# Kernel tuning notes

Hardware: AMD Instinct MI355X
Metric: run time of the kernel (lower is better)

Reference implementation:

```python
import jax, jax.numpy as jnp
import numpy as np

B, S, T = 64, 48, 48
E, H = 512, 1024
V_SRC, V_TGT = 32000, 32000
PAD = 0


def setup_inputs() -> dict:
    key = jax.random.key(0)
    ks = jax.random.split(key, 24)
    def g(k, shape, scale=0.05):
        return jax.random.normal(k, shape, dtype=jnp.float32) * scale
    return {
        "src_ids": jax.random.randint(ks[0], (S, B), 0, V_SRC),
        "tgt_ids": jax.random.randint(ks[1], (T, B), 0, V_TGT),
        "src_lengths": S,
        "src_emb": g(ks[2], (V_SRC, E)).at[PAD].set(0.0),
        "tgt_emb": g(ks[3], (V_TGT, E)).at[PAD].set(0.0),
        "cnn_w": g(ks[4], (E, E, 2)),
        "cnn_b": g(ks[5], (E,)),
        "enc_Wih_f": g(ks[6], (4 * H, E)),
        "enc_Whh_f": g(ks[7], (4 * H, H)),
        "enc_bih_f": g(ks[8], (4 * H,)),
        "enc_bhh_f": g(ks[9], (4 * H,)),
        "enc_Wih_b": g(ks[10], (4 * H, E)),
        "enc_Whh_b": g(ks[11], (4 * H, H)),
        "enc_bih_b": g(ks[12], (4 * H,)),
        "enc_bhh_b": g(ks[13], (4 * H,)),
        "dec_Wih": g(ks[14], (4 * H, E + H)),
        "dec_Whh": g(ks[15], (4 * H, H)),
        "dec_bih": g(ks[16], (4 * H,)),
        "dec_bhh": g(ks[17], (4 * H,)),
        "Wh": g(ks[18], (H, 2 * H)),
        "Wc": g(ks[19], (H, 2 * H)),
        "Watt": g(ks[20], (H, 2 * H)),
        "Wcomb": g(ks[21], (H, 3 * H)),
        "Wvocab": g(ks[22], (V_TGT, H)),
    }


def _lstm_cell(x, h, c, Wih, Whh, bih, bhh):
    gates = x @ Wih.T + h @ Whh.T + bih + bhh  # (b, 4h)
    i, f, g, o = jnp.split(gates, 4, axis=-1)
    c_new = jax.nn.sigmoid(f) * c + jax.nn.sigmoid(i) * jnp.tanh(g)
    h_new = jax.nn.sigmoid(o) * jnp.tanh(c_new)
    return h_new, c_new


def _forward(src_ids, tgt_ids,
             src_emb, tgt_emb, cnn_w, cnn_b,
             enc_Wih_f, enc_Whh_f, enc_bih_f, enc_bhh_f,
             enc_Wih_b, enc_Whh_b, enc_bih_b, enc_bhh_b,
             dec_Wih, dec_Whh, dec_bih, dec_bhh,
             Wh, Wc, Watt, Wcomb, Wvocab):
    b = src_ids.shape[1]
    h = Wh.shape[0]
    # ---- encode ----
    X = src_emb[src_ids]                       # (S, b, E)
    Xc = jnp.transpose(X, (1, 2, 0))           # (b, E, S)
    # Conv1d kernel_size=2, padding='same' in torch pads (left=0, right=1)
    Xc = jax.lax.conv_general_dilated(Xc, cnn_w, window_strides=(1,),
                                      padding=[(0, 1)],
                                      dimension_numbers=("NCH", "OIH", "NCH"))
    Xc = Xc + cnn_b[None, :, None]
    X = jnp.transpose(Xc, (2, 0, 1))           # (S, b, E)

    h0 = jnp.zeros((b, h), dtype=X.dtype)
    def fstep(carry, x_t):
        hh, cc = carry
        hh, cc = _lstm_cell(x_t, hh, cc, enc_Wih_f, enc_Whh_f, enc_bih_f, enc_bhh_f)
        return (hh, cc), hh
    def bstep(carry, x_t):
        hh, cc = carry
        hh, cc = _lstm_cell(x_t, hh, cc, enc_Wih_b, enc_Whh_b, enc_bih_b, enc_bhh_b)
        return (hh, cc), hh
    (hf, cf), out_f = jax.lax.scan(fstep, (h0, h0), X)
    (hb, cb), out_b = jax.lax.scan(bstep, (h0, h0), X[::-1])
    out_b = out_b[::-1]
    enc_hiddens = jnp.concatenate([out_f, out_b], axis=-1)   # (S, b, 2h)
    enc_hiddens = jnp.transpose(enc_hiddens, (1, 0, 2))      # (b, S, 2h)
    dec_h = jnp.concatenate([hf, hb], axis=1) @ Wh.T         # (b, h)
    dec_c = jnp.concatenate([cf, cb], axis=1) @ Wc.T         # (b, h)

    # ---- decode ----
    enc_proj = enc_hiddens @ Watt.T            # (b, S, h)
    enc_mask = jnp.zeros((b, enc_hiddens.shape[1]), dtype=bool)  # all full length
    Y = tgt_emb[tgt_ids[:-1]]                  # (T-1, b, E)

    def dstep(carry, Y_t):
        hh, cc, o_prev = carry
        ybar = jnp.concatenate([o_prev, Y_t], axis=1)        # (b, h+E)
        hh, cc = _lstm_cell(ybar, hh, cc, dec_Wih, dec_Whh, dec_bih, dec_bhh)
        e_t = jnp.einsum("bh,bsh->bs", hh, enc_proj)
        e_t = jnp.where(enc_mask, -jnp.inf, e_t)
        alpha = jax.nn.softmax(e_t, axis=-1)
        a_t = jnp.einsum("bs,bsd->bd", alpha, enc_hiddens)   # (b, 2h)
        O_t = jnp.tanh(jnp.concatenate([a_t, hh], axis=1) @ Wcomb.T)  # dropout rate 0
        return (hh, cc, O_t), O_t

    o0 = jnp.zeros((b, h), dtype=X.dtype)
    _, combined = jax.lax.scan(dstep, (dec_h, dec_c, o0), Y)  # (T-1, b, h)

    P = jax.nn.log_softmax(combined @ Wvocab.T, axis=-1)      # (T-1, b, V)
    gold = tgt_ids[1:]                                        # (T-1, b)
    logp = jnp.take_along_axis(P, gold[..., None], axis=-1)[..., 0]
    tmask = (gold != PAD).astype(P.dtype)
    return (logp * tmask).sum(axis=0)                         # (b,)


def reference(src_ids, tgt_ids, src_lengths,
              src_emb, tgt_emb, cnn_w, cnn_b,
              enc_Wih_f, enc_Whh_f, enc_bih_f, enc_bhh_f,
              enc_Wih_b, enc_Whh_b, enc_bih_b, enc_bhh_b,
              dec_Wih, dec_Whh, dec_bih, dec_bhh,
              Wh, Wc, Watt, Wcomb, Wvocab):
    # src_lengths == S for every sentence (packed seq degenerates to full-length LSTM)
    return _forward(src_ids, tgt_ids, src_emb, tgt_emb, cnn_w, cnn_b,
                    enc_Wih_f, enc_Whh_f, enc_bih_f, enc_bhh_f,
                    enc_Wih_b, enc_Whh_b, enc_bih_b, enc_bhh_b,
                    dec_Wih, dec_Whh, dec_bih, dec_bhh,
                    Wh, Wc, Watt, Wcomb, Wvocab)
```

## Files before the change

### kernel.cpp

```cpp
#include <hip/hip_runtime.h>
#include <hip/hip_bf16.h>
#include <math.h>

using f32x4 = __attribute__((ext_vector_type(4))) float;
using s16x8 = __attribute__((ext_vector_type(8))) short;
typedef unsigned short u16;
typedef unsigned int u32;
typedef unsigned long long u64;

#define MFMA16(a,b,c) __builtin_amdgcn_mfma_f32_16x16x32_bf16(a,b,c,0,0,0)
#define SCOPE_A __HIP_MEMORY_SCOPE_AGENT

__device__ __forceinline__ float bf2f(u16 u){
  union { u32 i; float f; } v; v.i = ((u32)u) << 16; return v.f;
}
__device__ __forceinline__ u16 f2bf(float f){
  union { float f; u32 i; } v; v.f = f;
  u32 x = v.i;
  return (u16)((x + 0x7fffu + ((x >> 16) & 1u)) >> 16);
}
__device__ __forceinline__ float sigm(float x){ return 1.0f/(1.0f + expf(-x)); }

__device__ __forceinline__ s16x8 pack8(const float* p){
  s16x8 r;
  #pragma unroll
  for (int i = 0; i < 8; ++i) r[i] = (short)f2bf(p[i]);
  return r;
}

__device__ __forceinline__ void coh_st32(void* p, u32 v){
  __hip_atomic_store((u32*)p, v, __ATOMIC_RELAXED, SCOPE_A);
}
__device__ __forceinline__ float u2f(u32 u){ union { u32 i; float f; } v; v.i = u; return v.f; }
__device__ __forceinline__ u32 f2u(float f){ union { float f; u32 i; } v; v.f = f; return v.i; }

__device__ __forceinline__ void poll(const int* flags, int n, int gen){
  for (int i = threadIdx.x; i < n; i += 256)
    while (__hip_atomic_load(flags + i, __ATOMIC_RELAXED, SCOPE_A) < gen)
      __builtin_amdgcn_s_sleep(1);
  __syncthreads();
}
__device__ __forceinline__ void setflag(int* flag, int gen){
  __syncthreads();
  if (threadIdx.x == 0)
    __hip_atomic_store(flag, gen, __ATOMIC_RELAXED, SCOPE_A);
}

__device__ __forceinline__ void gemm_k1024(
    const u16* ap, const char* wb0, const char* wb1, int xo, int addb,
    f32x4& a0, f32x4& a1)
{
  #pragma unroll
  for (int c = 0; c < 2; ++c){
    s16x8 st[16];
    #pragma unroll
    for (int q = 0; q < 16; ++q) st[q] = *(const s16x8*)(ap + c*512 + q*32);
    #pragma unroll
    for (int q = 0; q < 16; ++q){
      int cb = (addb + (c*512 + q*32)*2) ^ xo;
      a0 = MFMA16(st[q], *(const s16x8*)(wb0 + cb), a0);
      a1 = MFMA16(st[q], *(const s16x8*)(wb1 + cb), a1);
    }
  }
}

__global__ void k_zero(float* __restrict__ p, long n){
  long i = (long)blockIdx.x*blockDim.x + threadIdx.x;
  long st = (long)gridDim.x*blockDim.x;
  for (; i < n; i += st) p[i] = 0.0f;
}

__global__ void k_cast_bf16(const float* __restrict__ src, u16* __restrict__ dst, long n){
  long i = ((long)blockIdx.x*blockDim.x + threadIdx.x)*4;
  long st = (long)gridDim.x*blockDim.x*4;
  for (; i < n; i += st){
    float4 v = *(const float4*)(src + i);
    *(ushort4*)(dst + i) = make_ushort4(f2bf(v.x), f2bf(v.y), f2bf(v.z), f2bf(v.w));
  }
}

__global__ void k_addv(const float* __restrict__ a, const float* __restrict__ b,
                       float* __restrict__ d, int n){
  int i = blockIdx.x*blockDim.x + threadIdx.x;
  if (i < n) d[i] = a[i] + b[i];
}

__global__ void k_repack_conv(const float* __restrict__ w, u16* __restrict__ dst){
  int i = blockIdx.x*256 + threadIdx.x;
  int o = i >> 9, ii = i & 511;
  dst[(size_t)o*1024 + ii]       = f2bf(w[((size_t)o*512 + ii)*2 + 0]);
  dst[(size_t)o*1024 + 512 + ii] = f2bf(w[((size_t)o*512 + ii)*2 + 1]);
}

__global__ void k_build_wy(const float* __restrict__ dWih, u16* __restrict__ Wy){
  int i = blockIdx.x*256 + threadIdx.x;
  int r = i >> 9, c = i & 511;
  Wy[(size_t)r*512 + c] = f2bf(dWih[(size_t)r*1536 + 1024 + c]);
}

__global__ void k_split_wcomb(const float* __restrict__ Wcomb,
                              u16* __restrict__ Wca, u16* __restrict__ Whp){
  int r = blockIdx.x;
  for (int c = threadIdx.x; c < 2048; c += 256)
    Wca[(size_t)r*2048 + c] = f2bf(Wcomb[(size_t)r*3072 + c]);
  for (int c = threadIdx.x; c < 1024; c += 256)
    Whp[(size_t)r*1024 + c] = f2bf(Wcomb[(size_t)r*3072 + 2048 + c]);
}

__global__ void k_gather_src(const int* __restrict__ ids, const float* __restrict__ emb,
                             u16* __restrict__ Aconv){
  int s = blockIdx.x;
  int b = blockIdx.y;
  int e = threadIdx.x*4;
  float4 v = make_float4(0.f,0.f,0.f,0.f);
  if (s < 48){ int id = ids[s*64 + b]; v = *(const float4*)(emb + (size_t)id*512 + e); }
  ushort4 u = make_ushort4(f2bf(v.x), f2bf(v.y), f2bf(v.z), f2bf(v.w));
  if (s < 48) *(ushort4*)(Aconv + ((size_t)(s*64 + b))*1024 + e) = u;
  if (s >= 1) *(ushort4*)(Aconv + ((size_t)((s-1)*64 + b))*1024 + 512 + e) = u;
}

__global__ void k_gather_y(const int* __restrict__ ids, const float* __restrict__ emb,
                           u16* __restrict__ Y){
  int t = blockIdx.x; int b = blockIdx.y; int e = threadIdx.x*4;
  int id = ids[t*64 + b];
  float4 v = *(const float4*)(emb + (size_t)id*512 + e);
  *(ushort4*)(Y + ((size_t)(t*64 + b))*512 + e) = make_ushort4(f2bf(v.x), f2bf(v.y), f2bf(v.z), f2bf(v.w));
}

template<bool OUT_BF16, bool PACKG>
__global__ __launch_bounds__(256) void k_gemm(
    const u16* __restrict__ A0, long lda0,
    const u16* __restrict__ A1, long lda1, int ksplit,
    const u16* __restrict__ W, int K,
    void* __restrict__ Out, long ldc,
    const float* __restrict__ bias)
{
  __shared__ __align__(16) u16 As[64][72];
  __shared__ __align__(16) u16 Ws[64][72];
  const int t = threadIdx.x;
  const int m0 = blockIdx.x*64, n0 = blockIdx.y*64;
  const int w = t >> 6, l = t & 63, lr = l & 15, lh = l >> 4;
  const int sr = t >> 2, sk = (t & 3) << 4;

  f32x4 acc[4] = {{0,0,0,0},{0,0,0,0},{0,0,0,0},{0,0,0,0}};

  for (int kc = 0; kc < K; kc += 64){
    {
      const u16* wp = W + (size_t)(n0 + sr)*K + kc + sk;
      *(s16x8*)&Ws[sr][sk]     = *(const s16x8*)wp;
      *(s16x8*)&Ws[sr][sk + 8] = *(const s16x8*)(wp + 8);
    }
    {
      const u16* ap = (kc < ksplit)
        ? A0 + (size_t)(m0 + sr)*lda0 + kc
        : A1 + (size_t)(m0 + sr)*lda1 + (kc - ksplit);
      ap += sk;
      *(s16x8*)&As[sr][sk]     = *(const s16x8*)ap;
      *(s16x8*)&As[sr][sk + 8] = *(const s16x8*)(ap + 8);
    }
    __syncthreads();
    #pragma unroll
    for (int kk = 0; kk < 64; kk += 32){
      s16x8 a = *(const s16x8*)&As[w*16 + lr][kk + lh*8];
      #pragma unroll
      for (int ct = 0; ct < 4; ++ct){
        s16x8 bfr = *(const s16x8*)&Ws[ct*16 + lr][kk + lh*8];
        acc[ct] = MFMA16(a, bfr, acc[ct]);
      }
    }
    __syncthreads();
  }
  #pragma unroll
  for (int ct = 0; ct < 4; ++ct){
    #pragma unroll
    for (int rr = 0; rr < 4; ++rr){
      long row = m0 + w*16 + lh*4 + rr;
      long col = n0 + ct*16 + lr;
      float v = acc[ct][rr];
      if (bias) v += bias[col];
      if (PACKG){
        long time = row >> 6, b = row & 63, g = col >> 10, j = col & 1023;
        ((u16*)Out)[((time*1024 + j)*4 + g)*64 + b] = f2bf(v);
      } else {
        long oi = row*ldc + col;
        if (OUT_BF16) ((u16*)Out)[oi] = f2bf(v);
        else          ((float*)Out)[oi] = v;
      }
    }
  }
}

__global__ __launch_bounds__(256) void k_enc_persist(
    const float* __restrict__ WhhF, const float* __restrict__ WhhB,
    const u16* __restrict__ GfP, const u16* __restrict__ GbP,
    u16* __restrict__ hEF, u16* __restrict__ hEB,
    const u16* __restrict__ hzero,
    float* __restrict__ cF, float* __restrict__ cB,
    u16* __restrict__ Aatt, u16* __restrict__ cfbf, u16* __restrict__ cbbf,
    int* Eflags,
    const u16* __restrict__ Ybf, const u16* __restrict__ WyBf,
    const float* __restrict__ bdec, u16* __restrict__ GyP,
    const float* __restrict__ Wv, u16* __restrict__ WvBf)
{
  extern __shared__ char smem[];
  const int t = threadIdx.x, blk = blockIdx.x;
  const int w = t >> 6, l = t & 63, lr = l & 15, lh = l >> 4;

  if (blk >= 128){
    const int hb = blk - 128;
    u16 (*As)[72] = (u16(*)[72])smem;
    u16 (*Ws)[72] = (u16(*)[72])(smem + 64*72*2);
    const int sr = t >> 2, sk = (t & 3) << 4;
    for (int tile = hb; tile < 47*64; tile += 128){
      int m0 = (tile % 47)*64, n0 = (tile / 47)*64;
      f32x4 acc[4] = {{0,0,0,0},{0,0,0,0},{0,0,0,0},{0,0,0,0}};
      for (int kc = 0; kc < 512; kc += 64){
        const u16* wp = WyBf + (size_t)(n0 + sr)*512 + kc + sk;
        *(s16x8*)&Ws[sr][sk]     = *(const s16x8*)wp;
        *(s16x8*)&Ws[sr][sk + 8] = *(const s16x8*)(wp + 8);
        const u16* ap = Ybf + (size_t)(m0 + sr)*512 + kc + sk;
        *(s16x8*)&As[sr][sk]     = *(const s16x8*)ap;
        *(s16x8*)&As[sr][sk + 8] = *(const s16x8*)(ap + 8);
        __syncthreads();
        #pragma unroll
        for (int kk = 0; kk < 64; kk += 32){
          s16x8 a = *(const s16x8*)&As[w*16 + lr][kk + lh*8];
          #pragma unroll
          for (int ct = 0; ct < 4; ++ct){
            s16x8 bfr = *(const s16x8*)&Ws[ct*16 + lr][kk + lh*8];
            acc[ct] = MFMA16(a, bfr, acc[ct]);
          }
        }
        __syncthreads();
      }
      #pragma unroll
      for (int ct = 0; ct < 4; ++ct){
        #pragma unroll
        for (int rr = 0; rr < 4; ++rr){
          long row = m0 + w*16 + lh*4 + rr;
          long col = n0 + ct*16 + lr;
          float v = acc[ct][rr] + bdec[col];
          long time = row >> 6, b = row & 63, g = col >> 10, j = col & 1023;
          GyP[((time*1024 + j)*4 + g)*64 + b] = f2bf(v);
        }
      }
    }
    for (long i = ((long)hb*256 + t)*4; i < (long)32000*1024; i += (long)128*256*4){
      float4 v = *(const float4*)(Wv + i);
      *(ushort4*)(WvBf + i) = make_ushort4(f2bf(v.x), f2bf(v.y), f2bf(v.z), f2bf(v.w));
    }
    return;
  }

  const int dir = blk >> 6;
  const int j0 = (blk & 63) << 4;
  const float* Wsrc = dir ? WhhB : WhhF;
  const u16* GP = dir ? GbP : GfP;
  float* c = dir ? cB : cF;
  u16* cobf = dir ? cbbf : cfbf;
  u16* hE = dir ? hEB : hEF;
  int* myflags = Eflags + dir*64;
  const int myidx = blk & 63;

  for (int q = t; q < 64*128; q += 256){
    int row = q >> 7;
    int ck = (q & 127) << 3;
    int wrow = ((row >> 4)*1024) + j0 + (row & 15);
    s16x8 pk = pack8(Wsrc + (size_t)wrow*1024 + ck);
    *(s16x8*)(smem + row*2048 + ((ck*2) ^ ((row & 7) << 4))) = pk;
  }
  __syncthreads();

  const int lane_m = w*16 + lr;
  const int koff = lh*8;
  const char* wp0 = smem + lr*2048;
  const char* wp1 = smem + (16 + lr)*2048;
  const char* wp2 = smem + (32 + lr)*2048;
  const char* wp3 = smem + (48 + lr)*2048;
  const int xo = (lr & 7) << 4;
  const int j = j0 + lr;

  for (int s = 0; s < 48; ++s){
    const u16* hin = s ? (hE + (size_t)(s - 1)*65536) : hzero;
    u16* hout      = hE + (size_t)s*65536;
    const int time = dir ? 47 - s : s;
    if (s) poll(myflags, 64, s);
    f32x4 a0 = {0,0,0,0}, a1 = {0,0,0,0}, a2 = {0,0,0,0}, a3 = {0,0,0,0};
    const u16* ap = hin + (size_t)lane_m*1024 + koff;
    #pragma unroll
    for (int cc = 0; cc < 2; ++cc){
      s16x8 st[16];
      #pragma unroll
      for (int q = 0; q < 16; ++q) st[q] = *(const s16x8*)(ap + cc*512 + q*32);
      #pragma unroll
      for (int q = 0; q < 16; ++q){
        int cb = ((cc*512 + q*32 + koff)*2) ^ xo;
        a0 = MFMA16(st[q], *(const s16x8*)(wp0 + cb), a0);
        a1 = MFMA16(st[q], *(const s16x8*)(wp1 + cb), a1);
        a2 = MFMA16(st[q], *(const s16x8*)(wp2 + cb), a2);
        a3 = MFMA16(st[q], *(const s16x8*)(wp3 + cb), a3);
      }
    }
    #pragma unroll
    for (int rr = 0; rr < 4; ++rr){
      int b = w*16 + lh*4 + rr;
      const u16* gp = GP + (((size_t)time*1024 + j)*4)*64 + b;
      float gi = a0[rr] + bf2f(gp[0]);
      float gf = a1[rr] + bf2f(gp[64]);
      float gg = a2[rr] + bf2f(gp[128]);
      float go = a3[rr] + bf2f(gp[192]);
      float cn = sigm(gf)*c[b*1024 + j] + sigm(gi)*tanhf(gg);
      float hn = sigm(go)*tanhf(cn);
      c[b*1024 + j] = cn;
      u16 hb = f2bf(hn);
      u32 hi2 = __shfl_down((u32)hb, 1);
      if ((lr & 1) == 0)
        coh_st32((u32*)hout + ((b*1024 + j) >> 1), (u32)hb | (hi2 << 16));
      Aatt[((size_t)b*48 + time)*2048 + dir*1024 + j] = hb;
      if (s == 47) cobf[b*1024 + j] = f2bf(cn);
    }
    setflag(myflags + myidx, s + 1);
  }
}

__global__ __launch_bounds__(256) void k_dec_persist(
    const float* __restrict__ dWih, const float* __restrict__ dWhh,
    const u16* __restrict__ GyP,
    const u16* __restrict__ encP, const u16* __restrict__ encWc,
    const u16* __restrict__ Whp,
    const u16* __restrict__ hbinit, u16* __restrict__ hD,
    float* __restrict__ cdec,
    float* __restrict__ hp, u16* __restrict__ Cbf,
    const u16* __restrict__ obf_zero,
    int* Gflags, int* G2flags, int* Cflags)
{
  extern __shared__ char smem[];
  const int t = threadIdx.x, blk = blockIdx.x;
  const int w = t >> 6, l = t & 63, lr = l & 15, lh = l >> 4;
  const int lane_m = w*16 + lr;
  const int koff = lh*8;
  const int xo = (lr & 7) << 4;

  if (blk < 128){
    const int j0 = blk << 3;
    for (int q = t; q < 32*256; q += 256){
      int row = q >> 8;
      int ck = (q & 255) << 3;
      int wrow = ((row >> 3)*1024) + j0 + (row & 7);
      const float* src = (ck < 1024) ? dWih + (size_t)wrow*1536 + ck
                                     : dWhh + (size_t)wrow*1024 + (ck - 1024);
      s16x8 pk = pack8(src);
      *(s16x8*)(smem + row*4096 + ((ck*2) ^ ((row & 7) << 4))) = pk;
    }
    char* WhpL = smem + 131072;
    for (int q = t; q < 8*128; q += 256){
      int row = q >> 7, ck = (q & 127) << 3;
      s16x8 v = *(const s16x8*)(Whp + (size_t)(j0 + row)*1024 + ck);
      *(s16x8*)(WhpL + row*2048 + ((ck*2) ^ ((row & 7) << 4))) = v;
    }
    __syncthreads();
    const char* wp0 = smem + lr*4096;
    const char* wp1 = smem + (16 + lr)*4096;
    const char* wph = WhpL + (lr & 7)*2048;
    const int jj = lr & 7, gsel = lr >> 3;
    const int j = j0 + jj;

    s16x8 hreg[32];
    {
      const u16* ap = hbinit + (size_t)lane_m*1024 + koff;
      #pragma unroll
      for (int q = 0; q < 32; ++q) hreg[q] = *(const s16x8*)(ap + q*32);
    }

    for (int tt = 0; tt < 47; ++tt){
      u16* hout = hD + (size_t)tt*65536;
      f32x4 a0 = {0,0,0,0}, a1 = {0,0,0,0};
      #pragma unroll
      for (int q = 0; q < 32; ++q){
        int cb = ((1024 + q*32 + koff)*2) ^ xo;
        a0 = MFMA16(hreg[q], *(const s16x8*)(wp0 + cb), a0);
        a1 = MFMA16(hreg[q], *(const s16x8*)(wp1 + cb), a1);
      }
      if (tt) poll(Cflags, 64, tt);
      const u16* Ao = tt ? (Cbf + (size_t)(tt - 1)*65536) : obf_zero;
      gemm_k1024(Ao + (size_t)lane_m*1024 + koff, wp0, wp1, xo, koff*2, a0, a1);
      #pragma unroll
      for (int rr = 0; rr < 4; ++rr){
        float v0 = a0[rr], v1 = a1[rr];
        float p0 = __shfl_xor(v0, 8, 64);
        float p1 = __shfl_xor(v1, 8, 64);
        if (gsel == 0){
          int b = w*16 + lh*4 + rr;
          const u16* gp = GyP + (((size_t)tt*1024 + j)*4)*64 + b;
          float gi = v0 + bf2f(gp[0]);
          float gf = p0 + bf2f(gp[64]);
          float gg = v1 + bf2f(gp[128]);
          float go = p1 + bf2f(gp[192]);
          float cn = sigm(gf)*cdec[b*1024 + j] + sigm(gi)*tanhf(gg);
          float hn = sigm(go)*tanhf(cn);
          cdec[b*1024 + j] = cn;
          u16 hb = f2bf(hn);
          u32 hi2 = __shfl_down((u32)hb, 1);
          if ((jj & 1) == 0)
            coh_st32((u32*)hout + ((b*1024 + j) >> 1), (u32)hb | (hi2 << 16));
        }
      }
      setflag(Gflags + blk, tt + 1);
      poll(Gflags, 128, tt + 1);
      {
        const u16* ap = hout + (size_t)lane_m*1024 + koff;
        #pragma unroll
        for (int q = 0; q < 32; ++q) hreg[q] = *(const s16x8*)(ap + q*32);
      }
      f32x4 hpacc = {0,0,0,0};
      #pragma unroll
      for (int q = 0; q < 32; ++q){
        int cb = ((q*32 + koff)*2) ^ xo;
        s16x8 bw = {0,0,0,0,0,0,0,0};
        if (lr < 8) bw = *(const s16x8*)(wph + cb);
        hpacc = MFMA16(hreg[q], bw, hpacc);
      }
      if (lr < 8){
        float* hpout = hp + (size_t)tt*65536;
        #pragma unroll
        for (int rr = 0; rr < 4; ++rr)
          coh_st32(&hpout[(size_t)(w*16 + lh*4 + rr)*1024 + j0 + lr], f2u(hpacc[rr]));
      }
      setflag(G2flags + blk, tt + 1);
    }
  } else {
    const int b = blk - 128;
    u16* encPL = (u16*)smem;
    float* hs  = (float*)(smem + 98304);
    float* es  = (float*)(smem + 102400);
    float* al  = es + 48;
    float* sred= al + 48;
    for (int q = t; q < 48*128; q += 256){
      int row = q >> 7, ck = (q & 127) << 3;
      *(s16x8*)&encPL[row*1024 + ck] =
        *(const s16x8*)(encP + ((size_t)b*48 + row)*1024 + ck);
    }
    __syncthreads();

    for (int tt = 0; tt < 47; ++tt){
      poll(Gflags, 128, tt + 1);
      const u16* hrow = hD + (size_t)tt*65536 + (size_t)b*1024;
      {
        ushort4 v4 = ((const ushort4*)hrow)[t];
        hs[4*t]     = bf2f(v4.x);
        hs[4*t + 1] = bf2f(v4.y);
        hs[4*t + 2] = bf2f(v4.z);
        hs[4*t + 3] = bf2f(v4.w);
      }
      __syncthreads();
      for (int s2 = w; s2 < 48; s2 += 4){
        float p = 0.f;
        #pragma unroll
        for (int i = 0; i < 16; ++i)
          p += hs[l + 64*i]*bf2f(encPL[s2*1024 + l + 64*i]);
        #pragma unroll
        for (int d = 32; d >= 1; d >>= 1) p += __shfl_xor(p, d, 64);
        if (l == 0) es[s2] = p;
      }
      __syncthreads();
      if (t == 0){
        float m = es[0];
        for (int s2 = 1; s2 < 48; ++s2) m = fmaxf(m, es[s2]);
        float su = 0.f;
        for (int s2 = 0; s2 < 48; ++s2) su += expf(es[s2] - m);
        sred[0] = m; sred[1] = 1.0f/su;
      }
      __syncthreads();
      if (t < 48) al[t] = expf(es[t] - sred[0])*sred[1];
      __syncthreads();
      poll(G2flags, 128, tt + 1);
      int c0 = t*4;
      float4 hpv = *(const float4*)(hp + (size_t)tt*65536 + (size_t)b*1024 + c0);
      float acc0 = 0.f, acc1 = 0.f, acc2 = 0.f, acc3 = 0.f;
      const u16* ew = encWc + (size_t)b*48*1024 + c0;
      #pragma unroll 4
      for (int s2 = 0; s2 < 48; ++s2){
        float wgt = al[s2];
        ushort4 e4 = *(const ushort4*)(ew + (size_t)s2*1024);
        acc0 += wgt*bf2f(e4.x); acc1 += wgt*bf2f(e4.y);
        acc2 += wgt*bf2f(e4.z); acc3 += wgt*bf2f(e4.w);
      }
      float v0 = tanhf(hpv.x + acc0), v1 = tanhf(hpv.y + acc1);
      float v2 = tanhf(hpv.z + acc2), v3 = tanhf(hpv.w + acc3);
      size_t oi = (size_t)tt*65536 + (size_t)b*1024 + c0;
      coh_st32((u32*)Cbf + (oi >> 1),     (u32)f2bf(v0) | ((u32)f2bf(v1) << 16));
      coh_st32((u32*)Cbf + (oi >> 1) + 1, (u32)f2bf(v2) | ((u32)f2bf(v3) << 16));
      setflag(Cflags + b, tt + 1);
    }
  }
}

#define VNS 25
__global__ __launch_bounds__(256) void k_vocab_lse(
    const u16* __restrict__ Cbf, const u16* __restrict__ Wv, float2* __restrict__ partials)
{
  __shared__ __align__(16) u16 As[128][72];
  __shared__ __align__(16) u16 Bs[128][72];
  __shared__ float2 mg[128][2];
  int rb = blockIdx.x, sp = blockIdx.y;
  int m0 = rb*128;
  int t = threadIdx.x, w = t >> 6, l = t & 63, lr = l & 15, lh = l >> 4;
  int wr = w >> 1, wc = w & 1;
  int sr = t >> 1, sk = (t & 1) << 5;

  float mrun[4][4], srun[4][4];
  #pragma unroll
  for (int m = 0; m < 4; ++m)
    #pragma unroll
    for (int rr = 0; rr < 4; ++rr){ mrun[m][rr] = -INFINITY; srun[m][rr] = 0.f; }

  for (int nt = 0; nt < 10; ++nt){
    int n0 = sp*1280 + nt*128;
    f32x4 acc[4][4];
    #pragma unroll
    for (int m = 0; m < 4; ++m)
      #pragma unroll
      for (int n = 0; n < 4; ++n) acc[m][n] = (f32x4){0,0,0,0};

    for (int kc = 0; kc < 1024; kc += 64){
      int ar = m0 + sr; if (ar > 3007) ar = 3007;
      const u16* ap = Cbf + (size_t)ar*1024 + kc + sk;
      const u16* wp = Wv + (size_t)(n0 + sr)*1024 + kc + sk;
      #pragma unroll
      for (int q = 0; q < 4; ++q){
        *(s16x8*)&As[sr][sk + q*8] = *(const s16x8*)(ap + q*8);
        *(s16x8*)&Bs[sr][sk + q*8] = *(const s16x8*)(wp + q*8);
      }
      __syncthreads();
      #pragma unroll
      for (int kk = 0; kk < 64; kk += 32){
        s16x8 af[4], bf[4];
        #pragma unroll
        for (int m = 0; m < 4; ++m)
          af[m] = *(const s16x8*)&As[wr*64 + m*16 + lr][kk + lh*8];
        #pragma unroll
        for (int n = 0; n < 4; ++n)
          bf[n] = *(const s16x8*)&Bs[wc*64 + n*16 + lr][kk + lh*8];
        #pragma unroll
        for (int m = 0; m < 4; ++m)
          #pragma unroll
          for (int n = 0; n < 4; ++n)
            acc[m][n] = MFMA16(af[m], bf[n], acc[m][n]);
      }
      __syncthreads();
    }
    #pragma unroll
    for (int m = 0; m < 4; ++m){
      #pragma unroll
      for (int rr = 0; rr < 4; ++rr){
        float tm = fmaxf(fmaxf(acc[m][0][rr], acc[m][1][rr]),
                         fmaxf(acc[m][2][rr], acc[m][3][rr]));
        #pragma unroll
        for (int d = 1; d < 16; d <<= 1) tm = fmaxf(tm, __shfl_xor(tm, d, 64));
        float ts = expf(acc[m][0][rr] - tm) + expf(acc[m][1][rr] - tm)
                 + expf(acc[m][2][rr] - tm) + expf(acc[m][3][rr] - tm);
        #pragma unroll
        for (int d = 1; d < 16; d <<= 1) ts += __shfl_xor(ts, d, 64);
        if (tm > mrun[m][rr]){ srun[m][rr] = srun[m][rr]*expf(mrun[m][rr] - tm) + ts; mrun[m][rr] = tm; }
        else srun[m][rr] += ts*expf(tm - mrun[m][rr]);
      }
    }
  }
  __syncthreads();
  if (lr == 0){
    #pragma unroll
    for (int m = 0; m < 4; ++m)
      #pragma unroll
      for (int rr = 0; rr < 4; ++rr)
        mg[wr*64 + m*16 + lh*4 + rr][wc] = make_float2(mrun[m][rr], srun[m][rr]);
  }
  __syncthreads();
  if (t < 128){
    float2 p0 = mg[t][0], p1 = mg[t][1];
    float m = fmaxf(p0.x, p1.x);
    float s = p0.y*expf(p0.x - m) + p1.y*expf(p1.x - m);
    long row = m0 + t;
    if (row < 3008) partials[row*VNS + sp] = make_float2(m, s);
  }
}

__global__ void k_lse(const float2* __restrict__ partials, float* __restrict__ lse){
  int r = blockIdx.x*256 + threadIdx.x;
  if (r >= 3008) return;
  float m = -INFINITY, s = 0.f;
  for (int i = 0; i < VNS; ++i){
    float2 p = partials[r*VNS + i];
    if (p.x > m){ s = s*expf(m - p.x) + p.y; m = p.x; }
    else s += p.y*expf(p.x - m);
  }
  lse[r] = m + logf(s);
}

__global__ __launch_bounds__(256) void k_gold(const u16* __restrict__ Cbf,
                                              const u16* __restrict__ Wv,
                                              const int* __restrict__ tgt,
                                              float* __restrict__ gold){
  int w = threadIdx.x >> 6, l = threadIdx.x & 63;
  int r = blockIdx.x*4 + w;
  int tt = r >> 6, b = r & 63;
  int gid = tgt[(tt + 1)*64 + b];
  const u16* cp = Cbf + (size_t)r*1024;
  const u16* wp = Wv + (size_t)gid*1024;
  float p = 0.f;
  for (int i = l; i < 1024; i += 64) p += bf2f(cp[i])*bf2f(wp[i]);
  for (int d = 32; d >= 1; d >>= 1) p += __shfl_xor(p, d, 64);
  if (l == 0) gold[r] = p;
}

__global__ void k_final(const float* __restrict__ gold, const float* __restrict__ lse,
                        const int* __restrict__ tgt, float* __restrict__ out){
  int b = threadIdx.x;
  if (b >= 64) return;
  float acc = 0.f;
  for (int t = 0; t < 47; ++t){
    int gid = tgt[(t + 1)*64 + b];
    if (gid != 0) acc += gold[t*64 + b] - lse[t*64 + b];
  }
  out[b] = acc;
}

extern "C" void kernel_launch(void* const* d_in, const int* in_sizes, int n_in,
                              void* d_out, int out_size, void* d_ws, size_t ws_size,
                              hipStream_t stream)
{
  (void)in_sizes; (void)n_in; (void)out_size; (void)ws_size;
  const int*   src_ids = (const int*)d_in[0];
  const int*   tgt_ids = (const int*)d_in[1];
  const float* src_emb = (const float*)d_in[3];
  const float* tgt_emb = (const float*)d_in[4];
  const float* cnn_w   = (const float*)d_in[5];
  const float* cnn_b   = (const float*)d_in[6];
  const float* eWih_f  = (const float*)d_in[7];
  const float* eWhh_f  = (const float*)d_in[8];
  const float* ebih_f  = (const float*)d_in[9];
  const float* ebhh_f  = (const float*)d_in[10];
  const float* eWih_b  = (const float*)d_in[11];
  const float* eWhh_b  = (const float*)d_in[12];
  const float* ebih_b  = (const float*)d_in[13];
  const float* ebhh_b  = (const float*)d_in[14];
  const float* dWih    = (const float*)d_in[15];
  const float* dWhh    = (const float*)d_in[16];
  const float* dbih    = (const float*)d_in[17];
  const float* dbhh    = (const float*)d_in[18];
  const float* Wh      = (const float*)d_in[19];
  const float* Wc      = (const float*)d_in[20];
  const float* Watt    = (const float*)d_in[21];
  const float* Wcomb   = (const float*)d_in[22];
  const float* Wvocab  = (const float*)d_in[23];

  char* ws = (char*)d_ws;
  size_t off = 0;
  auto alloc = [&](size_t bytes)->char*{
    char* p = ws + off;
    off = (off + bytes + 255) & ~(size_t)255;
    return p;
  };

  float* cF     = (float*)alloc((size_t)65536*4);
  float* cB     = (float*)alloc((size_t)65536*4);
  u16* obf_zero = (u16*)alloc((size_t)65536*2);
  int* bar      = (int*)alloc(4096);
  size_t zero_floats = ((size_t)262144*2 + 131072 + 4096)/4;
  int* Eflags  = bar;
  int* Gflags  = bar + 128;
  int* G2flags = bar + 256;
  int* Cflags  = bar + 384;

  u16* Wconv_bf = (u16*)alloc((size_t)512*1024*2);
  u16* Wih_f_bf = (u16*)alloc((size_t)4096*512*2);
  u16* Wih_b_bf = (u16*)alloc((size_t)4096*512*2);
  u16* Wy_bf    = (u16*)alloc((size_t)4096*512*2);
  u16* Wh_bf    = (u16*)alloc((size_t)1024*2048*2);
  u16* Wc_bf    = (u16*)alloc((size_t)1024*2048*2);
  u16* Watt_bf  = (u16*)alloc((size_t)1024*2048*2);
  u16* Wca_bf   = (u16*)alloc((size_t)1024*2048*2);
  u16* Whp_bf   = (u16*)alloc((size_t)1024*1024*2);
  u16* Wv_bf    = (u16*)alloc((size_t)32000*1024*2);
  float* benc_f = (float*)alloc(4096*4);
  float* benc_b = (float*)alloc(4096*4);
  float* bdec   = (float*)alloc(4096*4);

  u16* Aconv    = (u16*)alloc((size_t)3072*1024*2);
  u16* Xc       = (u16*)alloc((size_t)3072*512*2);
  u16* GfP      = (u16*)alloc((size_t)48*1024*256*2);
  u16* GbP      = (u16*)alloc((size_t)48*1024*256*2);
  u16* GyP      = (u16*)alloc((size_t)47*1024*256*2);
  u16* Ybf      = (u16*)alloc((size_t)3008*512*2);
  u16* Aatt     = (u16*)alloc((size_t)3072*2048*2);
  u16* encP     = (u16*)alloc((size_t)3072*1024*2);
  u16* encWc    = (u16*)alloc((size_t)3072*1024*2);
  u16* hEF      = (u16*)alloc((size_t)48*65536*2);
  u16* hEB      = (u16*)alloc((size_t)48*65536*2);
  u16* cfbf     = (u16*)alloc((size_t)65536*2);
  u16* cbbf     = (u16*)alloc((size_t)65536*2);
  u16* hbinit   = (u16*)alloc((size_t)65536*2);
  u16* hD       = (u16*)alloc((size_t)47*65536*2);
  float* cdec   = (float*)alloc((size_t)65536*4);
  float* hp     = (float*)alloc((size_t)47*65536*4);
  u16* Cbf      = (u16*)alloc((size_t)3008*1024*2);
  float2* partials=(float2*)alloc((size_t)3008*VNS*8);
  float* lse    = (float*)alloc(3008*4);
  float* gold   = (float*)alloc(3008*4);

  k_zero<<<256, 256, 0, stream>>>(cF, (long)zero_floats);

  auto cgrid = [](long n)->int{ long g = (n/4 + 255)/256; return (int)(g > 1024 ? 1024 : g); };
  k_cast_bf16<<<cgrid(4096*512), 256, 0, stream>>>(eWih_f, Wih_f_bf, (long)4096*512);
  k_cast_bf16<<<cgrid(4096*512), 256, 0, stream>>>(eWih_b, Wih_b_bf, (long)4096*512);
  k_cast_bf16<<<cgrid(1024*2048), 256, 0, stream>>>(Wh, Wh_bf, (long)1024*2048);
  k_cast_bf16<<<cgrid(1024*2048), 256, 0, stream>>>(Wc, Wc_bf, (long)1024*2048);
  k_cast_bf16<<<cgrid(1024*2048), 256, 0, stream>>>(Watt, Watt_bf, (long)1024*2048);

  k_addv<<<16, 256, 0, stream>>>(ebih_f, ebhh_f, benc_f, 4096);
  k_addv<<<16, 256, 0, stream>>>(ebih_b, ebhh_b, benc_b, 4096);
  k_addv<<<16, 256, 0, stream>>>(dbih, dbhh, bdec, 4096);

  k_repack_conv<<<1024, 256, 0, stream>>>(cnn_w, Wconv_bf);
  k_build_wy<<<8192, 256, 0, stream>>>(dWih, Wy_bf);
  k_split_wcomb<<<1024, 256, 0, stream>>>(Wcomb, Wca_bf, Whp_bf);

  k_gather_src<<<dim3(49, 64), 128, 0, stream>>>(src_ids, src_emb, Aconv);
  k_gather_y<<<dim3(47, 64), 128, 0, stream>>>(tgt_ids, tgt_emb, Ybf);

  k_gemm<true, false><<<dim3(48, 8), 256, 0, stream>>>(
      Aconv, 1024, Aconv, 1024, 1024, Wconv_bf, 1024, Xc, 512, cnn_b);
  k_gemm<true, true><<<dim3(48, 64), 256, 0, stream>>>(
      Xc, 512, Xc, 512, 512, Wih_f_bf, 512, GfP, 0, benc_f);
  k_gemm<true, true><<<dim3(48, 64), 256, 0, stream>>>(
      Xc, 512, Xc, 512, 512, Wih_b_bf, 512, GbP, 0, benc_b);

  k_enc_persist<<<256, 256, 131072, stream>>>(
      eWhh_f, eWhh_b, GfP, GbP, hEF, hEB, obf_zero, cF, cB,
      Aatt, cfbf, cbbf, Eflags,
      Ybf, Wy_bf, bdec, GyP, Wvocab, Wv_bf);

  k_gemm<true, false><<<dim3(1, 16), 256, 0, stream>>>(
      hEF + (size_t)47*65536, 1024, hEB + (size_t)47*65536, 1024, 1024,
      Wh_bf, 2048, hbinit, 1024, nullptr);
  k_gemm<false, false><<<dim3(1, 16), 256, 0, stream>>>(
      cfbf, 1024, cbbf, 1024, 1024, Wc_bf, 2048, cdec, 1024, nullptr);
  k_gemm<true, false><<<dim3(48, 16), 256, 0, stream>>>(
      Aatt, 2048, Aatt, 2048, 2048, Watt_bf, 2048, encP, 1024, nullptr);
  k_gemm<true, false><<<dim3(48, 16), 256, 0, stream>>>(
      Aatt, 2048, Aatt, 2048, 2048, Wca_bf, 2048, encWc, 1024, nullptr);

  k_dec_persist<<<192, 256, 147456, stream>>>(
      dWih, dWhh, GyP, encP, encWc, Whp_bf, hbinit, hD, cdec,
      hp, Cbf, obf_zero, Gflags, G2flags, Cflags);

  k_vocab_lse<<<dim3(24, VNS), 256, 0, stream>>>(Cbf, Wv_bf, partials);
  k_lse<<<12, 256, 0, stream>>>(partials, lse);
  k_gold<<<752, 256, 0, stream>>>(Cbf, Wv_bf, tgt_ids, gold);
  k_final<<<1, 64, 0, stream>>>(gold, lse, tgt_ids, (float*)d_out);
}
```

Before: 2.769 ms.

## Pad sync flags to separate cache lines, store hp as bf16, warp-level softmax

Each inter-block flag now sits 16 ints (64 bytes) apart, so the flags set and polled by different blocks no longer share cache lines. This is meant to cut contention between spinning pollers and writers in the persistent encoder and decoder loops. The hp intermediate is now stored as packed bf16 rather than fp32, halving its traffic, at the cost of some precision. The single-thread softmax over 48 scores is replaced by wavefront shuffle reductions, which also removes one __syncthreads per step.

```diff
diff --git a/kernel.cpp b/kernel.cpp
--- a/kernel.cpp
+++ b/kernel.cpp
@@ -10,6 +10,7 @@
 
 #define MFMA16(a,b,c) __builtin_amdgcn_mfma_f32_16x16x32_bf16(a,b,c,0,0,0)
 #define SCOPE_A __HIP_MEMORY_SCOPE_AGENT
+#define FP 16
 
 __device__ __forceinline__ float bf2f(u16 u){
   union { u32 i; float f; } v; v.i = ((u32)u) << 16; return v.f;
@@ -36,7 +37,7 @@
 
 __device__ __forceinline__ void poll(const int* flags, int n, int gen){
   for (int i = threadIdx.x; i < n; i += 256)
-    while (__hip_atomic_load(flags + i, __ATOMIC_RELAXED, SCOPE_A) < gen)
+    while (__hip_atomic_load(flags + i*FP, __ATOMIC_RELAXED, SCOPE_A) < gen)
       __builtin_amdgcn_s_sleep(1);
   __syncthreads();
 }
@@ -259,7 +260,7 @@
   float* c = dir ? cB : cF;
   u16* cobf = dir ? cbbf : cfbf;
   u16* hE = dir ? hEB : hEF;
-  int* myflags = Eflags + dir*64;
+  int* myflags = Eflags + dir*64*FP;
   const int myidx = blk & 63;
 
   for (int q = t; q < 64*128; q += 256){
@@ -319,7 +320,7 @@
       Aatt[((size_t)b*48 + time)*2048 + dir*1024 + j] = hb;
       if (s == 47) cobf[b*1024 + j] = f2bf(cn);
     }
-    setflag(myflags + myidx, s + 1);
+    setflag(myflags + myidx*FP, s + 1);
   }
 }
 
@@ -330,7 +331,7 @@
     const u16* __restrict__ Whp,
     const u16* __restrict__ hbinit, u16* __restrict__ hD,
     float* __restrict__ cdec,
-    float* __restrict__ hp, u16* __restrict__ Cbf,
+    u16* __restrict__ hp, u16* __restrict__ Cbf,
     const u16* __restrict__ obf_zero,
     int* Gflags, int* G2flags, int* Cflags)
 {
@@ -405,7 +406,7 @@
             coh_st32((u32*)hout + ((b*1024 + j) >> 1), (u32)hb | (hi2 << 16));
         }
       }
-      setflag(Gflags + blk, tt + 1);
+      setflag(Gflags + blk*FP, tt + 1);
       poll(Gflags, 128, tt + 1);
       {
         const u16* ap = hout + (size_t)lane_m*1024 + koff;
@@ -421,12 +422,17 @@
         hpacc = MFMA16(hreg[q], bw, hpacc);
       }
       if (lr < 8){
-        float* hpout = hp + (size_t)tt*65536;
-        #pragma unroll
-        for (int rr = 0; rr < 4; ++rr)
-          coh_st32(&hpout[(size_t)(w*16 + lh*4 + rr)*1024 + j0 + lr], f2u(hpacc[rr]));
-      }
-      setflag(G2flags + blk, tt + 1);
+        u16* hpout = hp + (size_t)tt*65536;
+        #pragma unroll
+        for (int rr = 0; rr < 4; ++rr){
+          u16 hb = f2bf(hpacc[rr]);
+          u32 hi2 = __shfl_down((u32)hb, 1);
+          if ((lr & 1) == 0)
+            coh_st32((u32*)hpout + (((size_t)(w*16 + lh*4 + rr)*1024 + j0 + lr) >> 1),
+                     (u32)hb | (hi2 << 16));
+        }
+      }
+      setflag(G2flags + blk*FP, tt + 1);
     }
   } else {
     const int b = blk - 128;
@@ -434,7 +440,6 @@
     float* hs  = (float*)(smem + 98304);
     float* es  = (float*)(smem + 102400);
     float* al  = es + 48;
-    float* sred= al + 48;
     for (int q = t; q < 48*128; q += 256){
       int row = q >> 7, ck = (q & 127) << 3;
       *(s16x8*)&encPL[row*1024 + ck] =
@@ -463,19 +468,21 @@
         if (l == 0) es[s2] = p;
       }
       __syncthreads();
-      if (t == 0){
-        float m = es[0];
-        for (int s2 = 1; s2 < 48; ++s2) m = fmaxf(m, es[s2]);
-        float su = 0.f;
-        for (int s2 = 0; s2 < 48; ++s2) su += expf(es[s2] - m);
-        sred[0] = m; sred[1] = 1.0f/su;
-      }
-      __syncthreads();
-      if (t < 48) al[t] = expf(es[t] - sred[0])*sred[1];
+      if (w == 0){
+        float e = (l < 48) ? es[l] : -INFINITY;
+        float m = e;
+        #pragma unroll
+        for (int d = 32; d >= 1; d >>= 1) m = fmaxf(m, __shfl_xor(m, d, 64));
+        float ex = (l < 48) ? expf(e - m) : 0.f;
+        float su = ex;
+        #pragma unroll
+        for (int d = 32; d >= 1; d >>= 1) su += __shfl_xor(su, d, 64);
+        if (l < 48) al[l] = ex/su;
+      }
       __syncthreads();
       poll(G2flags, 128, tt + 1);
       int c0 = t*4;
-      float4 hpv = *(const float4*)(hp + (size_t)tt*65536 + (size_t)b*1024 + c0);
+      ushort4 h4 = *(const ushort4*)(hp + (size_t)tt*65536 + (size_t)b*1024 + c0);
       float acc0 = 0.f, acc1 = 0.f, acc2 = 0.f, acc3 = 0.f;
       const u16* ew = encWc + (size_t)b*48*1024 + c0;
       #pragma unroll 4
@@ -485,12 +492,12 @@
         acc0 += wgt*bf2f(e4.x); acc1 += wgt*bf2f(e4.y);
         acc2 += wgt*bf2f(e4.z); acc3 += wgt*bf2f(e4.w);
       }
-      float v0 = tanhf(hpv.x + acc0), v1 = tanhf(hpv.y + acc1);
-      float v2 = tanhf(hpv.z + acc2), v3 = tanhf(hpv.w + acc3);
+      float v0 = tanhf(bf2f(h4.x) + acc0), v1 = tanhf(bf2f(h4.y) + acc1);
+      float v2 = tanhf(bf2f(h4.z) + acc2), v3 = tanhf(bf2f(h4.w) + acc3);
       size_t oi = (size_t)tt*65536 + (size_t)b*1024 + c0;
       coh_st32((u32*)Cbf + (oi >> 1),     (u32)f2bf(v0) | ((u32)f2bf(v1) << 16));
       coh_st32((u32*)Cbf + (oi >> 1) + 1, (u32)f2bf(v2) | ((u32)f2bf(v3) << 16));
-      setflag(Cflags + b, tt + 1);
+      setflag(Cflags + b*FP, tt + 1);
     }
   }
 }
@@ -664,12 +671,12 @@
   float* cF     = (float*)alloc((size_t)65536*4);
   float* cB     = (float*)alloc((size_t)65536*4);
   u16* obf_zero = (u16*)alloc((size_t)65536*2);
-  int* bar      = (int*)alloc(4096);
-  size_t zero_floats = ((size_t)262144*2 + 131072 + 4096)/4;
+  int* bar      = (int*)alloc(32768);
+  size_t zero_floats = ((size_t)262144*2 + 131072 + 32768)/4;
   int* Eflags  = bar;
-  int* Gflags  = bar + 128;
-  int* G2flags = bar + 256;
-  int* Cflags  = bar + 384;
+  int* Gflags  = bar + 2048;
+  int* G2flags = bar + 4096;
+  int* Cflags  = bar + 6144;
 
   u16* Wconv_bf = (u16*)alloc((size_t)512*1024*2);
   u16* Wih_f_bf = (u16*)alloc((size_t)4096*512*2);
@@ -701,7 +708,7 @@
   u16* hbinit   = (u16*)alloc((size_t)65536*2);
   u16* hD       = (u16*)alloc((size_t)47*65536*2);
   float* cdec   = (float*)alloc((size_t)65536*4);
-  float* hp     = (float*)alloc((size_t)47*65536*4);
+  u16* hp       = (u16*)alloc((size_t)47*65536*2);
   u16* Cbf      = (u16*)alloc((size_t)3008*1024*2);
   float2* partials=(float2*)alloc((size_t)3008*VNS*8);
   float* lse    = (float*)alloc(3008*4);
```

Result: faster. 2.413 ms (-12.9%).
